# Performance work log

Hardware: AMD Instinct MI355X
Metric: run time of the kernel (lower is better)

The kernel has to match this reference:

```python
import jax, jax.numpy as jnp
import numpy as np

N_NODES = 10000
N_EDGES = 160000
IN_C, HID_C, OUT_C = 256, 512, 256
DROP_P = 0.5


def setup_inputs() -> dict:
    key = jax.random.key(0)
    ks = jax.random.split(key, 6)
    tensor = jax.random.normal(ks[0], (N_NODES, IN_C), dtype=jnp.float32)
    edge_index = jax.random.randint(ks[1], (2, N_EDGES), 0, N_NODES, dtype=jnp.int64)
    # Glorot-ish init for GCNConv linear weights, zero bias (PyG default bias init is zeros)
    W1 = jax.random.normal(ks[2], (IN_C, HID_C), dtype=jnp.float32) * (1.0 / np.sqrt(IN_C))
    b1 = jnp.zeros((HID_C,), dtype=jnp.float32)
    W2 = jax.random.normal(ks[3], (HID_C, OUT_C), dtype=jnp.float32) * (1.0 / np.sqrt(HID_C))
    b2 = jnp.zeros((OUT_C,), dtype=jnp.float32)
    return {"tensor": tensor, "edge_index": edge_index, "W1": W1, "b1": b1, "W2": W2, "b2": b2}


def _gcn_layer(x, W, b, src, dst, n_nodes):
    # x' = D^{-1/2} (A + I) D^{-1/2} X W + b  (PyG GCNConv, add_self_loops=True)
    xw = x @ W                                             # [N, C_out]
    deg = jax.ops.segment_sum(jnp.ones(src.shape[0], xw.dtype), dst,
                              num_segments=n_nodes)        # includes self-loops -> deg >= 1
    dinv = jax.lax.rsqrt(deg)
    norm = dinv[src] * dinv[dst]                           # [E+N]
    msg = xw[src] * norm[:, None]                          # gather + normalize
    out = jax.ops.segment_sum(msg, dst, num_segments=n_nodes)  # scatter-add
    return out + b


def _dropout(x, key, p):
    keep = jax.random.bernoulli(key, 1.0 - p, x.shape)
    return jnp.where(keep, x / (1.0 - p), jnp.zeros((), x.dtype))


def reference(tensor, edge_index, W1, b1, W2, b2):
    n = tensor.shape[0]
    src, dst = edge_index[0], edge_index[1]
    loops = jnp.arange(n, dtype=src.dtype)
    src_f = jnp.concatenate([src, loops])
    dst_f = jnp.concatenate([dst, loops])

    dk1, dk2 = jax.random.split(jax.random.key(42))
    h = _gcn_layer(tensor, W1, b1, src_f, dst_f, n)
    h = jax.nn.relu(h)
    h = _dropout(h, dk1, DROP_P)
    h = _gcn_layer(h, W2, b2, src_f, dst_f, n)
    h = jax.nn.relu(h)
    h = _dropout(h, dk2, DROP_P)
    return h
```

## Files before the change

kernel.cpp:

```cpp
#include <hip/hip_runtime.h>
#include <stdint.h>


#define C_IN 256
#define C_HID 512
#define C_OUT 256

typedef unsigned short ushort_t;
typedef __bf16 bf16x8 __attribute__((ext_vector_type(8)));
typedef float floatx4 __attribute__((ext_vector_type(4)));

__host__ __device__ __forceinline__ void tf_rounds(unsigned& x0, unsigned& x1,
                                                   unsigned k0, unsigned k1) {
  unsigned k2 = k0 ^ k1 ^ 0x1BD11BDAu;
#define ROT(r) { x0 += x1; x1 = (x1 << r) | (x1 >> (32 - r)); x1 ^= x0; }
  x0 += k0; x1 += k1;
  ROT(13) ROT(15) ROT(26) ROT(6)
  x0 += k1; x1 += k2 + 1u;
  ROT(17) ROT(29) ROT(16) ROT(24)
  x0 += k2; x1 += k0 + 2u;
  ROT(13) ROT(15) ROT(26) ROT(6)
  x0 += k0; x1 += k1 + 3u;
  ROT(17) ROT(29) ROT(16) ROT(24)
  x0 += k1; x1 += k2 + 4u;
  ROT(13) ROT(15) ROT(26) ROT(6)
  x0 += k2; x1 += k0 + 5u;
#undef ROT
}

__device__ __forceinline__ float drop_scale(unsigned j, unsigned k0, unsigned k1) {
  unsigned x0 = 0u, x1 = j;
  tf_rounds(x0, x1, k0, k1);
  unsigned bits = x0 ^ x1;
  float u = __uint_as_float((bits >> 9) | 0x3f800000u) - 1.0f;
  return (u < 0.5f) ? 2.0f : 0.0f;
}

__device__ __forceinline__ ushort_t f2bf(float f) {
  unsigned u = __float_as_uint(f);
  unsigned r = (u + 0x7fffu + ((u >> 16) & 1u)) >> 16;
  return (ushort_t)r;
}
__device__ __forceinline__ float bf2f(ushort_t h) {
  return __uint_as_float(((unsigned)h) << 16);
}

__global__ __launch_bounds__(256) void k_detect(const unsigned* __restrict__ raw,
                                                unsigned* flag, int nwords) {
  __shared__ unsigned sh[256];
  unsigned acc = 0;
  for (int i = 1 + 2 * (int)threadIdx.x; i < nwords; i += 512) acc |= raw[i];
  sh[threadIdx.x] = acc;
  __syncthreads();
  for (int s = 128; s > 0; s >>= 1) {
    if ((int)threadIdx.x < s) sh[threadIdx.x] |= sh[threadIdx.x + s];
    __syncthreads();
  }
  if (threadIdx.x == 0) *flag = (sh[0] == 0u) ? 1u : 0u;
}

__global__ __launch_bounds__(256) void k_zero(int* p, int n) {
  int i = blockIdx.x * 256 + threadIdx.x;
  if (i < n) p[i] = 0;
}

__global__ __launch_bounds__(256) void k_convert(const void* __restrict__ raw,
                                                 const unsigned* __restrict__ flag,
                                                 int* __restrict__ eic,
                                                 int* __restrict__ cnt,
                                                 int E) {
  int i = blockIdx.x * 256 + threadIdx.x;
  if (i >= 2 * E) return;
  int v;
  if (*flag) v = (int)((const long long*)raw)[i];
  else       v = ((const int*)raw)[i];
  eic[i] = v;
  if (i >= E) atomicAdd(&cnt[v], 1);
}

__global__ __launch_bounds__(256) void k_scan_a(const int* __restrict__ cnt,
                                                int* __restrict__ bsum, int n) {
  __shared__ int sh[256];
  int i = blockIdx.x * 256 + threadIdx.x;
  sh[threadIdx.x] = (i < n) ? cnt[i] : 0;
  __syncthreads();
  for (int s = 128; s > 0; s >>= 1) {
    if ((int)threadIdx.x < s) sh[threadIdx.x] += sh[threadIdx.x + s];
    __syncthreads();
  }
  if (threadIdx.x == 0) bsum[blockIdx.x] = sh[0];
}
__global__ __launch_bounds__(64) void k_scan_b(const int* __restrict__ bsum,
                                               int* __restrict__ boff,
                                               int* __restrict__ roff_last,
                                               int nb) {
  if (threadIdx.x == 0) {
    int run = 0;
    for (int b = 0; b < nb; ++b) { boff[b] = run; run += bsum[b]; }
    *roff_last = run;
  }
}
__global__ __launch_bounds__(256) void k_scan_c(const int* __restrict__ cnt,
                                                const int* __restrict__ boff,
                                                int* __restrict__ roff,
                                                int* __restrict__ cursor,
                                                float* __restrict__ dinv, int n) {
  __shared__ int sh[256];
  int i = blockIdx.x * 256 + threadIdx.x;
  int v = (i < n) ? cnt[i] : 0;
  sh[threadIdx.x] = v;
  __syncthreads();
  for (int s = 1; s < 256; s <<= 1) {
    int t = ((int)threadIdx.x >= s) ? sh[threadIdx.x - s] : 0;
    __syncthreads();
    sh[threadIdx.x] += t;
    __syncthreads();
  }
  if (i < n) {
    int excl = boff[blockIdx.x] + sh[threadIdx.x] - v;
    roff[i] = excl;
    cursor[i] = excl;
    dinv[i] = rsqrtf((float)(v + 1));
  }
}

__global__ __launch_bounds__(256) void k_scatter(const int* __restrict__ eic,
                                                 int* __restrict__ cursor,
                                                 int* __restrict__ csr, int E) {
  int e = blockIdx.x * 256 + threadIdx.x;
  if (e >= E) return;
  int s = eic[e], d = eic[E + e];
  int slot = atomicAdd(&cursor[d], 1);
  csr[slot] = s;
}

__global__ __launch_bounds__(256) void k_wconv2(const float* __restrict__ W1,
                                                const float* __restrict__ W2,
                                                ushort_t* __restrict__ h1,
                                                ushort_t* __restrict__ l1,
                                                ushort_t* __restrict__ h2,
                                                ushort_t* __restrict__ l2) {
  int idx = blockIdx.x * 256 + threadIdx.x;
  const int S1 = C_IN * C_HID;
  const float* W; ushort_t *hi, *lo; int K, Nn, li;
  if (idx < S1) { W = W1; hi = h1; lo = l1; K = C_IN; Nn = C_HID; li = idx; }
  else { W = W2; hi = h2; lo = l2; K = C_HID; Nn = C_OUT; li = idx - S1; }
  int k = li / Nn, n = li - k * Nn;
  float v = W[li];
  ushort_t h = f2bf(v);
  hi[(size_t)n * K + k] = h;
  lo[(size_t)n * K + k] = f2bf(v - bf2f(h));
}

template <int EPI>
__global__ __launch_bounds__(256) void k_gather4(const int* __restrict__ roff,
                                                 const int* __restrict__ csr,
                                                 const float* __restrict__ dinv,
                                                 const float* __restrict__ x,
                                                 const float* __restrict__ bias,
                                                 void* __restrict__ o1,
                                                 void* __restrict__ o2,
                                                 unsigned dk0, unsigned dk1) {
  int g = threadIdx.x >> 6;
  int tg = threadIdx.x & 63;
  int node = blockIdx.x * 4 + g;
  float dd = dinv[node];
  float4 v = ((const float4*)(x + (size_t)node * 256))[tg];
  float4 acc = make_float4(dd * v.x, dd * v.y, dd * v.z, dd * v.w);
  int p = roff[node], end = roff[node + 1];
  for (; p + 4 <= end; p += 4) {
    int s0 = csr[p], s1 = csr[p + 1], s2 = csr[p + 2], s3 = csr[p + 3];
    float w0 = dinv[s0], w1 = dinv[s1], w2 = dinv[s2], w3 = dinv[s3];
    float4 a = ((const float4*)(x + (size_t)s0 * 256))[tg];
    float4 b = ((const float4*)(x + (size_t)s1 * 256))[tg];
    float4 c = ((const float4*)(x + (size_t)s2 * 256))[tg];
    float4 d = ((const float4*)(x + (size_t)s3 * 256))[tg];
    acc.x += w0 * a.x + w1 * b.x + w2 * c.x + w3 * d.x;
    acc.y += w0 * a.y + w1 * b.y + w2 * c.y + w3 * d.y;
    acc.z += w0 * a.z + w1 * b.z + w2 * c.z + w3 * d.z;
    acc.w += w0 * a.w + w1 * b.w + w2 * c.w + w3 * d.w;
  }
  for (; p < end; ++p) {
    int s0 = csr[p];
    float w0 = dinv[s0];
    float4 a = ((const float4*)(x + (size_t)s0 * 256))[tg];
    acc.x += w0 * a.x; acc.y += w0 * a.y; acc.z += w0 * a.z; acc.w += w0 * a.w;
  }
  acc.x *= dd; acc.y *= dd; acc.z *= dd; acc.w *= dd;
  if (EPI) {
    float4 bb = ((const float4*)bias)[tg];
    acc.x = fmaxf(acc.x + bb.x, 0.0f);
    acc.y = fmaxf(acc.y + bb.y, 0.0f);
    acc.z = fmaxf(acc.z + bb.z, 0.0f);
    acc.w = fmaxf(acc.w + bb.w, 0.0f);
    unsigned jb = (unsigned)node * 256u + (unsigned)tg * 4u;
    acc.x *= drop_scale(jb + 0u, dk0, dk1);
    acc.y *= drop_scale(jb + 1u, dk0, dk1);
    acc.z *= drop_scale(jb + 2u, dk0, dk1);
    acc.w *= drop_scale(jb + 3u, dk0, dk1);
    ((float4*)o1)[(size_t)node * 64 + tg] = acc;
  } else {
    ushort_t h0 = f2bf(acc.x), h1 = f2bf(acc.y), h2 = f2bf(acc.z), h3 = f2bf(acc.w);
    ushort4 hv = make_ushort4(h0, h1, h2, h3);
    ushort4 lv = make_ushort4(f2bf(acc.x - bf2f(h0)), f2bf(acc.y - bf2f(h1)),
                              f2bf(acc.z - bf2f(h2)), f2bf(acc.w - bf2f(h3)));
    ((ushort4*)o1)[(size_t)node * 64 + tg] = hv;
    ((ushort4*)o2)[(size_t)node * 64 + tg] = lv;
  }
}

template <int EPI>
__global__ __launch_bounds__(256) void k_gemm3(
    const ushort_t* __restrict__ Ahi, const ushort_t* __restrict__ Alo,
    const ushort_t* __restrict__ Bhi, const ushort_t* __restrict__ Blo,
    const float* __restrict__ bias,
    ushort_t* __restrict__ Chi, ushort_t* __restrict__ Clo,
    float* __restrict__ Cf,
    int M, int N, int K, unsigned dk0, unsigned dk1) {
  __shared__ ushort_t sAh[128 * 32], sAl[128 * 32], sBh[128 * 32], sBl[128 * 32];
  const int t = threadIdx.x;
  const int lane = t & 63, wave = t >> 6;
  const int wm = wave & 1, wn = wave >> 1;
  const int quad = lane >> 4, l16 = lane & 15;
  const int row0 = blockIdx.y * 128, col0 = blockIdx.x * 128;
  const int srow = t >> 2;
  const int skc = (t & 3) * 8;

  floatx4 acc[4][4] = {};

  const int ra0 = min(row0 + srow, M - 1);
  const int ra1 = min(row0 + 64 + srow, M - 1);
  const int rb0 = col0 + srow;
  const int rb1 = col0 + 64 + srow;

  for (int kt = 0; kt < K; kt += 32) {
    const size_t ka = (size_t)kt + skc;
    uint4 vA0h = *(const uint4*)(Ahi + (size_t)ra0 * K + ka);
    uint4 vA1h = *(const uint4*)(Ahi + (size_t)ra1 * K + ka);
    uint4 vA0l = *(const uint4*)(Alo + (size_t)ra0 * K + ka);
    uint4 vA1l = *(const uint4*)(Alo + (size_t)ra1 * K + ka);
    uint4 vB0h = *(const uint4*)(Bhi + (size_t)rb0 * K + ka);
    uint4 vB1h = *(const uint4*)(Bhi + (size_t)rb1 * K + ka);
    uint4 vB0l = *(const uint4*)(Blo + (size_t)rb0 * K + ka);
    uint4 vB1l = *(const uint4*)(Blo + (size_t)rb1 * K + ka);
    __syncthreads();
    *(uint4*)&sAh[srow * 32 + skc] = vA0h;
    *(uint4*)&sAh[(64 + srow) * 32 + skc] = vA1h;
    *(uint4*)&sAl[srow * 32 + skc] = vA0l;
    *(uint4*)&sAl[(64 + srow) * 32 + skc] = vA1l;
    *(uint4*)&sBh[srow * 32 + skc] = vB0h;
    *(uint4*)&sBh[(64 + srow) * 32 + skc] = vB1h;
    *(uint4*)&sBl[srow * 32 + skc] = vB0l;
    *(uint4*)&sBl[(64 + srow) * 32 + skc] = vB1l;
    __syncthreads();

    bf16x8 ah[4], al[4], bh[4], bl[4];
#pragma unroll
    for (int i = 0; i < 4; ++i) {
      int off = (wm * 64 + i * 16 + l16) * 32 + quad * 8;
      ah[i] = *(const bf16x8*)&sAh[off];
      al[i] = *(const bf16x8*)&sAl[off];
    }
#pragma unroll
    for (int j = 0; j < 4; ++j) {
      int off = (wn * 64 + j * 16 + l16) * 32 + quad * 8;
      bh[j] = *(const bf16x8*)&sBh[off];
      bl[j] = *(const bf16x8*)&sBl[off];
    }
#pragma unroll
    for (int i = 0; i < 4; ++i)
#pragma unroll
      for (int j = 0; j < 4; ++j) {
        acc[i][j] = __builtin_amdgcn_mfma_f32_16x16x32_bf16(ah[i], bh[j], acc[i][j], 0, 0, 0);
        acc[i][j] = __builtin_amdgcn_mfma_f32_16x16x32_bf16(ah[i], bl[j], acc[i][j], 0, 0, 0);
        acc[i][j] = __builtin_amdgcn_mfma_f32_16x16x32_bf16(al[i], bh[j], acc[i][j], 0, 0, 0);
      }
  }

#pragma unroll
  for (int i = 0; i < 4; ++i) {
#pragma unroll
    for (int j = 0; j < 4; ++j) {
      int gc = col0 + wn * 64 + j * 16 + l16;
#pragma unroll
      for (int reg = 0; reg < 4; ++reg) {
        int gr = row0 + wm * 64 + i * 16 + quad * 4 + reg;
        if (gr >= M) continue;
        float v = acc[i][j][reg];
        size_t o = (size_t)gr * N + gc;
        if (EPI) {
          v += bias[gc];
          v = fmaxf(v, 0.0f);
          v *= drop_scale((unsigned)gr * (unsigned)N + (unsigned)gc, dk0, dk1);
          ushort_t h = f2bf(v);
          Chi[o] = h;
          Clo[o] = f2bf(v - bf2f(h));
        } else {
          Cf[o] = v;
        }
      }
    }
  }
}

extern "C" void kernel_launch(void* const* d_in, const int* in_sizes, int n_in,
                              void* d_out, int out_size, void* d_ws, size_t ws_size,
                              hipStream_t stream) {
  const float* x  = (const float*)d_in[0];
  const void*  ei = d_in[1];
  const float* W1 = (const float*)d_in[2];
  const float* b1 = (const float*)d_in[3];
  const float* W2 = (const float*)d_in[4];
  const float* b2 = (const float*)d_in[5];
  float* out = (float*)d_out;

  const int N = in_sizes[0] / C_IN;
  const int E = in_sizes[1] / 2;
  const int NB = (N + 255) / 256;

  unsigned a0 = 0u, a1 = 0u, b0 = 0u, b1k = 1u;
  tf_rounds(a0, a1, 0u, 42u);
  tf_rounds(b0, b1k, 0u, 42u);

  uintptr_t base = (uintptr_t)d_ws;
  unsigned*  flag   = (unsigned*)base;
  int*       bsum   = (int*)(base + 4096);
  int*       boff   = (int*)(base + 8192);
  int*       cnt    = (int*)(base + 16 * 1024);
  int*       roff   = (int*)(base + 64 * 1024);
  int*       cursor = (int*)(base + 128 * 1024);
  float*     dinv   = (float*)(base + 192 * 1024);
  int*       eic    = (int*)(base + 256 * 1024);
  int*       csr    = (int*)(base + 2u * 1024 * 1024);
  ushort_t*  Ahi    = (ushort_t*)(base + 4u  * 1024 * 1024);
  ushort_t*  Alo    = (ushort_t*)(base + 10u * 1024 * 1024);
  ushort_t*  H1hi   = (ushort_t*)(base + 16u * 1024 * 1024);
  ushort_t*  H1lo   = (ushort_t*)(base + 27u * 1024 * 1024);
  float*     hw2    = (float*)(base + 38u * 1024 * 1024);
  ushort_t*  W1thi  = (ushort_t*)(base + 49u * 1024 * 1024);
  ushort_t*  W1tlo  = (ushort_t*)(base + 49u * 1024 * 1024 + 512 * 1024);
  ushort_t*  W2thi  = (ushort_t*)(base + 50u * 1024 * 1024);
  ushort_t*  W2tlo  = (ushort_t*)(base + 50u * 1024 * 1024 + 512 * 1024);

  dim3 b256(256);
  k_detect<<<dim3(1), b256, 0, stream>>>((const unsigned*)ei, flag, 8192);
  k_zero<<<dim3(NB), b256, 0, stream>>>(cnt, N);
  k_convert<<<dim3((2 * E + 255) / 256), b256, 0, stream>>>(ei, flag, eic, cnt, E);
  k_scan_a<<<dim3(NB), b256, 0, stream>>>(cnt, bsum, N);
  k_scan_b<<<dim3(1), dim3(64), 0, stream>>>(bsum, boff, roff + N, NB);
  k_scan_c<<<dim3(NB), b256, 0, stream>>>(cnt, boff, roff, cursor, dinv, N);
  k_scatter<<<dim3((E + 255) / 256), b256, 0, stream>>>(eic, cursor, csr, E);
  k_wconv2<<<dim3((C_IN * C_HID + C_HID * C_OUT + 255) / 256), b256, 0, stream>>>(
      W1, W2, W1thi, W1tlo, W2thi, W2tlo);
  k_gather4<0><<<dim3(N / 4), b256, 0, stream>>>(roff, csr, dinv, x, nullptr,
                                                 Ahi, Alo, 0u, 0u);
  k_gemm3<1><<<dim3(C_HID / 128, (N + 127) / 128), b256, 0, stream>>>(
      Ahi, Alo, W1thi, W1tlo, b1, H1hi, H1lo, nullptr, N, C_HID, C_IN, a0, a1);
  k_gemm3<0><<<dim3(C_OUT / 128, (N + 127) / 128), b256, 0, stream>>>(
      H1hi, H1lo, W2thi, W2tlo, nullptr, nullptr, nullptr, hw2, N, C_OUT, C_HID, 0u, 0u);
  k_gather4<1><<<dim3(N / 4), b256, 0, stream>>>(roff, csr, dinv, hw2, b2,
                                                 out, nullptr, b0, b1k);
}
```

Before: 215.5 us.

## Fuse setup kernels, drop scan pass, prescale layer-2 rows, async LDS GEMM loads

Merges the zeroing, index-width detection and weight conversion into one launch, and removes the serial block-offset scan by having each scan block sum the preceding block totals itself. The second GEMM now multiplies rows by dinv, so the final gather skips per-edge dinv loads. The gather loop is unrolled to 8 edges for more memory parallelism. The GEMM tile is halved in M and switches to global_load_lds direct-to-LDS copies without register staging. The cost is more GEMM blocks, a single-buffered LDS tile with two barriers per step, and an in-block prefix that assumes at most 64 scan blocks.

```diff
diff --git a/kernel.cpp b/kernel.cpp
--- a/kernel.cpp
+++ b/kernel.cpp
@@ -9,6 +9,13 @@
 typedef unsigned short ushort_t;
 typedef __bf16 bf16x8 __attribute__((ext_vector_type(8)));
 typedef float floatx4 __attribute__((ext_vector_type(4)));
+
+typedef __attribute__((address_space(1))) const void g1_void;
+typedef __attribute__((address_space(3))) void l3_void;
+
+__device__ __forceinline__ void gll16(const ushort_t* g, ushort_t* l) {
+  __builtin_amdgcn_global_load_lds((g1_void*)g, (l3_void*)l, 16, 0, 0);
+}
 
 __host__ __device__ __forceinline__ void tf_rounds(unsigned& x0, unsigned& x1,
                                                    unsigned k0, unsigned k1) {
@@ -45,23 +52,45 @@
   return __uint_as_float(((unsigned)h) << 16);
 }
 
-__global__ __launch_bounds__(256) void k_detect(const unsigned* __restrict__ raw,
-                                                unsigned* flag, int nwords) {
-  __shared__ unsigned sh[256];
-  unsigned acc = 0;
-  for (int i = 1 + 2 * (int)threadIdx.x; i < nwords; i += 512) acc |= raw[i];
-  sh[threadIdx.x] = acc;
-  __syncthreads();
-  for (int s = 128; s > 0; s >>= 1) {
-    if ((int)threadIdx.x < s) sh[threadIdx.x] |= sh[threadIdx.x + s];
-    __syncthreads();
-  }
-  if (threadIdx.x == 0) *flag = (sh[0] == 0u) ? 1u : 0u;
-}
-
-__global__ __launch_bounds__(256) void k_zero(int* p, int n) {
-  int i = blockIdx.x * 256 + threadIdx.x;
-  if (i < n) p[i] = 0;
+__global__ __launch_bounds__(256) void k_setup(const unsigned* __restrict__ raw,
+                                               unsigned* __restrict__ flag,
+                                               int* __restrict__ cnt, int N, int NB,
+                                               const float* __restrict__ W1,
+                                               const float* __restrict__ W2,
+                                               ushort_t* __restrict__ h1,
+                                               ushort_t* __restrict__ l1,
+                                               ushort_t* __restrict__ h2,
+                                               ushort_t* __restrict__ l2) {
+  int b = blockIdx.x, t = threadIdx.x;
+  if (b < NB) {
+    int i = b * 256 + t;
+    if (i < N) cnt[i] = 0;
+    return;
+  }
+  if (b == NB) {
+    __shared__ unsigned sh[256];
+    unsigned acc = 0;
+    for (int i = 1 + 2 * t; i < 8192; i += 512) acc |= raw[i];
+    sh[t] = acc;
+    __syncthreads();
+    for (int s = 128; s > 0; s >>= 1) {
+      if (t < s) sh[t] |= sh[t + s];
+      __syncthreads();
+    }
+    if (t == 0) *flag = (sh[0] == 0u) ? 1u : 0u;
+    return;
+  }
+  int idx = (b - NB - 1) * 256 + t;
+  const int S1 = C_IN * C_HID;
+  if (idx >= S1 + C_HID * C_OUT) return;
+  const float* W; ushort_t *hi, *lo; int K, Nn, li;
+  if (idx < S1) { W = W1; hi = h1; lo = l1; K = C_IN; Nn = C_HID; li = idx; }
+  else { W = W2; hi = h2; lo = l2; K = C_HID; Nn = C_OUT; li = idx - S1; }
+  int k = li / Nn, n = li - k * Nn;
+  float v = W[li];
+  ushort_t h = f2bf(v);
+  hi[(size_t)n * K + k] = h;
+  lo[(size_t)n * K + k] = f2bf(v - bf2f(h));
 }
 
 __global__ __launch_bounds__(256) void k_convert(const void* __restrict__ raw,
@@ -90,38 +119,38 @@
   }
   if (threadIdx.x == 0) bsum[blockIdx.x] = sh[0];
 }
-__global__ __launch_bounds__(64) void k_scan_b(const int* __restrict__ bsum,
-                                               int* __restrict__ boff,
-                                               int* __restrict__ roff_last,
-                                               int nb) {
-  if (threadIdx.x == 0) {
-    int run = 0;
-    for (int b = 0; b < nb; ++b) { boff[b] = run; run += bsum[b]; }
-    *roff_last = run;
-  }
-}
+
 __global__ __launch_bounds__(256) void k_scan_c(const int* __restrict__ cnt,
-                                                const int* __restrict__ boff,
+                                                const int* __restrict__ bsum,
                                                 int* __restrict__ roff,
                                                 int* __restrict__ cursor,
-                                                float* __restrict__ dinv, int n) {
+                                                float* __restrict__ dinv,
+                                                int n, int NB, int E) {
   __shared__ int sh[256];
-  int i = blockIdx.x * 256 + threadIdx.x;
+  __shared__ int spre;
+  int t = threadIdx.x;
+  if (t < 64) {
+    int v = (t < (int)blockIdx.x && t < NB) ? bsum[t] : 0;
+    for (int s = 32; s > 0; s >>= 1) v += __shfl_down(v, s);
+    if (t == 0) spre = v;
+  }
+  int i = blockIdx.x * 256 + t;
   int v = (i < n) ? cnt[i] : 0;
-  sh[threadIdx.x] = v;
+  sh[t] = v;
   __syncthreads();
   for (int s = 1; s < 256; s <<= 1) {
-    int t = ((int)threadIdx.x >= s) ? sh[threadIdx.x - s] : 0;
-    __syncthreads();
-    sh[threadIdx.x] += t;
+    int tv = (t >= s) ? sh[t - s] : 0;
+    __syncthreads();
+    sh[t] += tv;
     __syncthreads();
   }
   if (i < n) {
-    int excl = boff[blockIdx.x] + sh[threadIdx.x] - v;
+    int excl = spre + sh[t] - v;
     roff[i] = excl;
     cursor[i] = excl;
     dinv[i] = rsqrtf((float)(v + 1));
   }
+  if (blockIdx.x == 0 && t == 0) roff[n] = E;
 }
 
 __global__ __launch_bounds__(256) void k_scatter(const int* __restrict__ eic,
@@ -134,25 +163,7 @@
   csr[slot] = s;
 }
 
-__global__ __launch_bounds__(256) void k_wconv2(const float* __restrict__ W1,
-                                                const float* __restrict__ W2,
-                                                ushort_t* __restrict__ h1,
-                                                ushort_t* __restrict__ l1,
-                                                ushort_t* __restrict__ h2,
-                                                ushort_t* __restrict__ l2) {
-  int idx = blockIdx.x * 256 + threadIdx.x;
-  const int S1 = C_IN * C_HID;
-  const float* W; ushort_t *hi, *lo; int K, Nn, li;
-  if (idx < S1) { W = W1; hi = h1; lo = l1; K = C_IN; Nn = C_HID; li = idx; }
-  else { W = W2; hi = h2; lo = l2; K = C_HID; Nn = C_OUT; li = idx - S1; }
-  int k = li / Nn, n = li - k * Nn;
-  float v = W[li];
-  ushort_t h = f2bf(v);
-  hi[(size_t)n * K + k] = h;
-  lo[(size_t)n * K + k] = f2bf(v - bf2f(h));
-}
-
-template <int EPI>
+template <int EPI, int PRE>
 __global__ __launch_bounds__(256) void k_gather4(const int* __restrict__ roff,
                                                  const int* __restrict__ csr,
                                                  const float* __restrict__ dinv,
@@ -165,26 +176,63 @@
   int tg = threadIdx.x & 63;
   int node = blockIdx.x * 4 + g;
   float dd = dinv[node];
-  float4 v = ((const float4*)(x + (size_t)node * 256))[tg];
-  float4 acc = make_float4(dd * v.x, dd * v.y, dd * v.z, dd * v.w);
+  const float4* xr = (const float4*)x;
+  float4 v = xr[(size_t)node * 64 + tg];
+  float4 acc;
+  if (PRE) acc = v;
+  else acc = make_float4(dd * v.x, dd * v.y, dd * v.z, dd * v.w);
   int p = roff[node], end = roff[node + 1];
+  for (; p + 8 <= end; p += 8) {
+    int s[8];
+#pragma unroll
+    for (int q = 0; q < 8; ++q) s[q] = csr[p + q];
+    float4 r[8];
+#pragma unroll
+    for (int q = 0; q < 8; ++q) r[q] = xr[(size_t)s[q] * 64 + tg];
+    if (PRE) {
+#pragma unroll
+      for (int q = 0; q < 8; ++q) {
+        acc.x += r[q].x; acc.y += r[q].y; acc.z += r[q].z; acc.w += r[q].w;
+      }
+    } else {
+      float w[8];
+#pragma unroll
+      for (int q = 0; q < 8; ++q) w[q] = dinv[s[q]];
+#pragma unroll
+      for (int q = 0; q < 8; ++q) {
+        acc.x += w[q] * r[q].x; acc.y += w[q] * r[q].y;
+        acc.z += w[q] * r[q].z; acc.w += w[q] * r[q].w;
+      }
+    }
+  }
   for (; p + 4 <= end; p += 4) {
     int s0 = csr[p], s1 = csr[p + 1], s2 = csr[p + 2], s3 = csr[p + 3];
-    float w0 = dinv[s0], w1 = dinv[s1], w2 = dinv[s2], w3 = dinv[s3];
-    float4 a = ((const float4*)(x + (size_t)s0 * 256))[tg];
-    float4 b = ((const float4*)(x + (size_t)s1 * 256))[tg];
-    float4 c = ((const float4*)(x + (size_t)s2 * 256))[tg];
-    float4 d = ((const float4*)(x + (size_t)s3 * 256))[tg];
-    acc.x += w0 * a.x + w1 * b.x + w2 * c.x + w3 * d.x;
-    acc.y += w0 * a.y + w1 * b.y + w2 * c.y + w3 * d.y;
-    acc.z += w0 * a.z + w1 * b.z + w2 * c.z + w3 * d.z;
-    acc.w += w0 * a.w + w1 * b.w + w2 * c.w + w3 * d.w;
+    float4 a = xr[(size_t)s0 * 64 + tg];
+    float4 b = xr[(size_t)s1 * 64 + tg];
+    float4 c = xr[(size_t)s2 * 64 + tg];
+    float4 d = xr[(size_t)s3 * 64 + tg];
+    if (PRE) {
+      acc.x += a.x + b.x + c.x + d.x;
+      acc.y += a.y + b.y + c.y + d.y;
+      acc.z += a.z + b.z + c.z + d.z;
+      acc.w += a.w + b.w + c.w + d.w;
+    } else {
+      float w0 = dinv[s0], w1 = dinv[s1], w2 = dinv[s2], w3 = dinv[s3];
+      acc.x += w0 * a.x + w1 * b.x + w2 * c.x + w3 * d.x;
+      acc.y += w0 * a.y + w1 * b.y + w2 * c.y + w3 * d.y;
+      acc.z += w0 * a.z + w1 * b.z + w2 * c.z + w3 * d.z;
+      acc.w += w0 * a.w + w1 * b.w + w2 * c.w + w3 * d.w;
+    }
   }
   for (; p < end; ++p) {
     int s0 = csr[p];
-    float w0 = dinv[s0];
-    float4 a = ((const float4*)(x + (size_t)s0 * 256))[tg];
-    acc.x += w0 * a.x; acc.y += w0 * a.y; acc.z += w0 * a.z; acc.w += w0 * a.w;
+    float4 a = xr[(size_t)s0 * 64 + tg];
+    if (PRE) {
+      acc.x += a.x; acc.y += a.y; acc.z += a.z; acc.w += a.w;
+    } else {
+      float w0 = dinv[s0];
+      acc.x += w0 * a.x; acc.y += w0 * a.y; acc.z += w0 * a.z; acc.w += w0 * a.w;
+    }
   }
   acc.x *= dd; acc.y *= dd; acc.z *= dd; acc.w *= dd;
   if (EPI) {
@@ -213,51 +261,51 @@
 __global__ __launch_bounds__(256) void k_gemm3(
     const ushort_t* __restrict__ Ahi, const ushort_t* __restrict__ Alo,
     const ushort_t* __restrict__ Bhi, const ushort_t* __restrict__ Blo,
-    const float* __restrict__ bias,
+    const float* __restrict__ bias, const float* __restrict__ dscale,
     ushort_t* __restrict__ Chi, ushort_t* __restrict__ Clo,
     float* __restrict__ Cf,
     int M, int N, int K, unsigned dk0, unsigned dk1) {
-  __shared__ ushort_t sAh[128 * 32], sAl[128 * 32], sBh[128 * 32], sBl[128 * 32];
+  __shared__ ushort_t sAh[64 * 32], sAl[64 * 32], sBh[128 * 32], sBl[128 * 32];
   const int t = threadIdx.x;
   const int lane = t & 63, wave = t >> 6;
   const int wm = wave & 1, wn = wave >> 1;
   const int quad = lane >> 4, l16 = lane & 15;
-  const int row0 = blockIdx.y * 128, col0 = blockIdx.x * 128;
+  const int row0 = blockIdx.y * 64, col0 = blockIdx.x * 128;
   const int srow = t >> 2;
   const int skc = (t & 3) * 8;
 
-  floatx4 acc[4][4] = {};
-
-  const int ra0 = min(row0 + srow, M - 1);
-  const int ra1 = min(row0 + 64 + srow, M - 1);
+  floatx4 acc[2][4] = {};
+
+  const int ra  = min(row0 + srow, M - 1);
   const int rb0 = col0 + srow;
   const int rb1 = col0 + 64 + srow;
 
+  const ushort_t* gAh = Ahi + (size_t)ra * K + skc;
+  const ushort_t* gAl = Alo + (size_t)ra * K + skc;
+  const ushort_t* gB0h = Bhi + (size_t)rb0 * K + skc;
+  const ushort_t* gB1h = Bhi + (size_t)rb1 * K + skc;
+  const ushort_t* gB0l = Blo + (size_t)rb0 * K + skc;
+  const ushort_t* gB1l = Blo + (size_t)rb1 * K + skc;
+  ushort_t* lAh = &sAh[wave * 512];
+  ushort_t* lAl = &sAl[wave * 512];
+  ushort_t* lB0h = &sBh[wave * 512];
+  ushort_t* lB1h = &sBh[2048 + wave * 512];
+  ushort_t* lB0l = &sBl[wave * 512];
+  ushort_t* lB1l = &sBl[2048 + wave * 512];
+
   for (int kt = 0; kt < K; kt += 32) {
-    const size_t ka = (size_t)kt + skc;
-    uint4 vA0h = *(const uint4*)(Ahi + (size_t)ra0 * K + ka);
-    uint4 vA1h = *(const uint4*)(Ahi + (size_t)ra1 * K + ka);
-    uint4 vA0l = *(const uint4*)(Alo + (size_t)ra0 * K + ka);
-    uint4 vA1l = *(const uint4*)(Alo + (size_t)ra1 * K + ka);
-    uint4 vB0h = *(const uint4*)(Bhi + (size_t)rb0 * K + ka);
-    uint4 vB1h = *(const uint4*)(Bhi + (size_t)rb1 * K + ka);
-    uint4 vB0l = *(const uint4*)(Blo + (size_t)rb0 * K + ka);
-    uint4 vB1l = *(const uint4*)(Blo + (size_t)rb1 * K + ka);
-    __syncthreads();
-    *(uint4*)&sAh[srow * 32 + skc] = vA0h;
-    *(uint4*)&sAh[(64 + srow) * 32 + skc] = vA1h;
-    *(uint4*)&sAl[srow * 32 + skc] = vA0l;
-    *(uint4*)&sAl[(64 + srow) * 32 + skc] = vA1l;
-    *(uint4*)&sBh[srow * 32 + skc] = vB0h;
-    *(uint4*)&sBh[(64 + srow) * 32 + skc] = vB1h;
-    *(uint4*)&sBl[srow * 32 + skc] = vB0l;
-    *(uint4*)&sBl[(64 + srow) * 32 + skc] = vB1l;
-    __syncthreads();
-
-    bf16x8 ah[4], al[4], bh[4], bl[4];
-#pragma unroll
-    for (int i = 0; i < 4; ++i) {
-      int off = (wm * 64 + i * 16 + l16) * 32 + quad * 8;
+    gll16(gAh + kt, lAh);
+    gll16(gAl + kt, lAl);
+    gll16(gB0h + kt, lB0h);
+    gll16(gB1h + kt, lB1h);
+    gll16(gB0l + kt, lB0l);
+    gll16(gB1l + kt, lB1l);
+    __syncthreads();
+
+    bf16x8 ah[2], al[2], bh[4], bl[4];
+#pragma unroll
+    for (int i = 0; i < 2; ++i) {
+      int off = (wm * 32 + i * 16 + l16) * 32 + quad * 8;
       ah[i] = *(const bf16x8*)&sAh[off];
       al[i] = *(const bf16x8*)&sAl[off];
     }
@@ -268,23 +316,24 @@
       bl[j] = *(const bf16x8*)&sBl[off];
     }
 #pragma unroll
-    for (int i = 0; i < 4; ++i)
+    for (int i = 0; i < 2; ++i)
 #pragma unroll
       for (int j = 0; j < 4; ++j) {
         acc[i][j] = __builtin_amdgcn_mfma_f32_16x16x32_bf16(ah[i], bh[j], acc[i][j], 0, 0, 0);
         acc[i][j] = __builtin_amdgcn_mfma_f32_16x16x32_bf16(ah[i], bl[j], acc[i][j], 0, 0, 0);
         acc[i][j] = __builtin_amdgcn_mfma_f32_16x16x32_bf16(al[i], bh[j], acc[i][j], 0, 0, 0);
       }
-  }
-
-#pragma unroll
-  for (int i = 0; i < 4; ++i) {
+    __syncthreads();
+  }
+
+#pragma unroll
+  for (int i = 0; i < 2; ++i) {
 #pragma unroll
     for (int j = 0; j < 4; ++j) {
       int gc = col0 + wn * 64 + j * 16 + l16;
 #pragma unroll
       for (int reg = 0; reg < 4; ++reg) {
-        int gr = row0 + wm * 64 + i * 16 + quad * 4 + reg;
+        int gr = row0 + wm * 32 + i * 16 + quad * 4 + reg;
         if (gr >= M) continue;
         float v = acc[i][j][reg];
         size_t o = (size_t)gr * N + gc;
@@ -296,7 +345,7 @@
           Chi[o] = h;
           Clo[o] = f2bf(v - bf2f(h));
         } else {
-          Cf[o] = v;
+          Cf[o] = v * dscale[gr];
         }
       }
     }
@@ -325,7 +374,6 @@
   uintptr_t base = (uintptr_t)d_ws;
   unsigned*  flag   = (unsigned*)base;
   int*       bsum   = (int*)(base + 4096);
-  int*       boff   = (int*)(base + 8192);
   int*       cnt    = (int*)(base + 16 * 1024);
   int*       roff   = (int*)(base + 64 * 1024);
   int*       cursor = (int*)(base + 128 * 1024);
@@ -343,21 +391,23 @@
   ushort_t*  W2tlo  = (ushort_t*)(base + 50u * 1024 * 1024 + 512 * 1024);
 
   dim3 b256(256);
-  k_detect<<<dim3(1), b256, 0, stream>>>((const unsigned*)ei, flag, 8192);
-  k_zero<<<dim3(NB), b256, 0, stream>>>(cnt, N);
+  const int WCB = (C_IN * C_HID + C_HID * C_OUT + 255) / 256;
+
+  k_setup<<<dim3(NB + 1 + WCB), b256, 0, stream>>>((const unsigned*)ei, flag, cnt,
+                                                   N, NB, W1, W2,
+                                                   W1thi, W1tlo, W2thi, W2tlo);
   k_convert<<<dim3((2 * E + 255) / 256), b256, 0, stream>>>(ei, flag, eic, cnt, E);
   k_scan_a<<<dim3(NB), b256, 0, stream>>>(cnt, bsum, N);
-  k_scan_b<<<dim3(1), dim3(64), 0, stream>>>(bsum, boff, roff + N, NB);
-  k_scan_c<<<dim3(NB), b256, 0, stream>>>(cnt, boff, roff, cursor, dinv, N);
+  k_scan_c<<<dim3(NB), b256, 0, stream>>>(cnt, bsum, roff, cursor, dinv, N, NB, E);
   k_scatter<<<dim3((E + 255) / 256), b256, 0, stream>>>(eic, cursor, csr, E);
-  k_wconv2<<<dim3((C_IN * C_HID + C_HID * C_OUT + 255) / 256), b256, 0, stream>>>(
-      W1, W2, W1thi, W1tlo, W2thi, W2tlo);
-  k_gather4<0><<<dim3(N / 4), b256, 0, stream>>>(roff, csr, dinv, x, nullptr,
-                                                 Ahi, Alo, 0u, 0u);
-  k_gemm3<1><<<dim3(C_HID / 128, (N + 127) / 128), b256, 0, stream>>>(
-      Ahi, Alo, W1thi, W1tlo, b1, H1hi, H1lo, nullptr, N, C_HID, C_IN, a0, a1);
-  k_gemm3<0><<<dim3(C_OUT / 128, (N + 127) / 128), b256, 0, stream>>>(
-      H1hi, H1lo, W2thi, W2tlo, nullptr, nullptr, nullptr, hw2, N, C_OUT, C_HID, 0u, 0u);
-  k_gather4<1><<<dim3(N / 4), b256, 0, stream>>>(roff, csr, dinv, hw2, b2,
-                                                 out, nullptr, b0, b1k);
-}
+  k_gather4<0, 0><<<dim3(N / 4), b256, 0, stream>>>(roff, csr, dinv, x, nullptr,
+                                                    Ahi, Alo, 0u, 0u);
+  k_gemm3<1><<<dim3(C_HID / 128, (N + 63) / 64), b256, 0, stream>>>(
+      Ahi, Alo, W1thi, W1tlo, b1, nullptr, H1hi, H1lo, nullptr,
+      N, C_HID, C_IN, a0, a1);
+  k_gemm3<0><<<dim3(C_OUT / 128, (N + 63) / 64), b256, 0, stream>>>(
+      H1hi, H1lo, W2thi, W2tlo, nullptr, dinv, nullptr, nullptr, hw2,
+      N, C_OUT, C_HID, 0u, 0u);
+  k_gather4<1, 1><<<dim3(N / 4), b256, 0, stream>>>(roff, csr, dinv, hw2, b2,
+                                                    out, nullptr, b0, b1k);
+}
```

New measurement: 198.7 us. -7.8%, faster.
